# Kernel tuning notes

Measured on AMD Instinct MI355X. Metric: run time of the kernel, lower is better.

Reference implementation:

```python
import jax, jax.numpy as jnp
import numpy as np

V = 25000
E = 100000
NODE_IN = 74
EDGE_IN = 12
OUT = 64
EHID = 128
NUM_STEPS = 6


def setup_inputs() -> dict:
    key = jax.random.key(0)
    ks = jax.random.split(key, 12)
    s = 0.05
    node_feats = jax.random.normal(ks[0], (V, NODE_IN), dtype=jnp.float32)
    edge_feats = jax.random.normal(ks[1], (E, EDGE_IN), dtype=jnp.float32)
    src = jax.random.randint(ks[2], (E,), 0, V)
    dst = jax.random.randint(ks[3], (E,), 0, V)
    # project_node_feats: Linear(node_in, out)
    Wp = jax.random.normal(ks[4], (NODE_IN, OUT), dtype=jnp.float32) * s
    bp = jnp.zeros((OUT,), dtype=jnp.float32)
    # edge network: Linear(edge_in, ehid) -> ReLU -> Linear(ehid, out*out)
    We1 = jax.random.normal(ks[5], (EDGE_IN, EHID), dtype=jnp.float32) * s
    be1 = jnp.zeros((EHID,), dtype=jnp.float32)
    We2 = jax.random.normal(ks[6], (EHID, OUT * OUT), dtype=jnp.float32) * s
    be2 = jnp.zeros((OUT * OUT,), dtype=jnp.float32)
    # NNConv output bias
    bias = jnp.zeros((OUT,), dtype=jnp.float32)
    return {
        "node_feats": node_feats, "edge_feats": edge_feats,
        "src": src, "dst": dst,
        "Wp": Wp, "bp": bp,
        "We1": We1, "be1": be1, "We2": We2, "be2": be2,
        "bias": bias,
    }


def reference(node_feats, edge_feats, src, dst, Wp, bp, We1, be1, We2, be2, bias):
    # project node features
    h = jax.nn.relu(node_feats @ Wp + bp)  # [V, OUT]
    # per-edge weight matrices (same every step -> hoist out of loop)
    ew = jax.nn.relu(edge_feats @ We1 + be1) @ We2 + be2  # [E, OUT*OUT]
    ew = ew.reshape(E, OUT, OUT)
    for _ in range(NUM_STEPS):
        # gather src node feats, batched matvec, scatter-sum to dst
        msg = jnp.einsum('ei,eio->eo', h[src], ew)  # [E, OUT]
        agg = jax.ops.segment_sum(msg, dst, num_segments=V)  # [V, OUT]
        h = jax.nn.relu(agg + bias)
    return h
```

## Files before the change

### kernel.cpp

```cpp
#include <hip/hip_runtime.h>
#include <hip/hip_bf16.h>

#define Vn 25000
#define En 100000
#define NODE_IN 74
#define EDGE_IN 12
#define OUTD 64
#define EHID 128
#define NUM_STEPS 6

typedef __attribute__((ext_vector_type(8))) short short8;
typedef __attribute__((ext_vector_type(4))) float floatx4;

__device__ __forceinline__ short f2bfbits(float x) {
  union { float fv; unsigned u; } c; c.fv = x;
  unsigned r = (c.u + 0x7fffu + ((c.u >> 16) & 1u)) >> 16;
  return (short)r;
}

__global__ void proj_kernel(const float* __restrict__ node,
                            const float* __restrict__ Wp,
                            const float* __restrict__ bp,
                            float* __restrict__ h) {
  __shared__ float nf[NODE_IN];
  int v = blockIdx.x;
  int o = threadIdx.x;
  for (int i = o; i < NODE_IN; i += 64) nf[i] = node[(size_t)v * NODE_IN + i];
  __syncthreads();
  float acc = bp[o];
  for (int i = 0; i < NODE_IN; ++i) acc = fmaf(nf[i], Wp[i * OUTD + o], acc);
  h[(size_t)v * OUTD + o] = fmaxf(acc, 0.0f);
}

__global__ void edge_kernel(const float* __restrict__ ef,
                            const float* __restrict__ We1,
                            const float* __restrict__ be1,
                            __hip_bfloat16* __restrict__ f) {
  __shared__ float es[EDGE_IN];
  int e = blockIdx.x;
  int k = threadIdx.x;
  if (k < EDGE_IN) es[k] = ef[(size_t)e * EDGE_IN + k];
  __syncthreads();
  float acc = be1[k];
  for (int j = 0; j < EDGE_IN; ++j) acc = fmaf(es[j], We1[j * EHID + k], acc);
  f[(size_t)e * EHID + k] = __float2bfloat16(fmaxf(acc, 0.0f));
}

__global__ void w2r_kernel(const float* __restrict__ We2,
                           __hip_bfloat16* __restrict__ w2s) {
  int g = blockIdx.x * 256 + threadIdx.x;
  int j = g & 7;
  int quad = (g >> 3) & 3;
  int l15 = (g >> 5) & 15;
  int s = (g >> 9) & 3;
  int wv = (g >> 11) & 3;
  int i = g >> 13;
  int k = s * 32 + quad * 8 + j;
  int col = i * 64 + wv * 16 + l15;
  w2s[g] = __float2bfloat16(We2[(size_t)k * (OUTD * OUTD) + col]);
}

__global__ __launch_bounds__(256) void msg_kernel(
    const float* __restrict__ h,
    const __hip_bfloat16* __restrict__ f,
    const __hip_bfloat16* __restrict__ w2s,
    const int* __restrict__ src,
    const int* __restrict__ dst,
    const float* __restrict__ be2,
    float* __restrict__ agg) {
  __shared__ float h_t[64 * 68];
  __shared__ int s_dst[64];

  const int tid = threadIdx.x;
  const int wv = tid >> 6;
  const int lane = tid & 63;
  const int quad = lane >> 4;
  const int l15 = lane & 15;
  const int e0 = blockIdx.x * 64;

  if (tid < 64) {
    int e = e0 + tid;
    s_dst[tid] = (e < En) ? dst[e] : -1;
  }
  {
    int e = tid & 63;
    int ib = tid >> 6;
    int eg = e0 + e;
    int sv = (eg < En) ? src[eg] : 0;
    const float4* hp = reinterpret_cast<const float4*>(h + (size_t)sv * OUTD + ib * 16);
    for (int c = 0; c < 4; ++c) {
      float4 val = hp[c];
      int ib4 = ib * 16 + c * 4;
      h_t[(ib4 + 0) * 68 + e] = val.x;
      h_t[(ib4 + 1) * 68 + e] = val.y;
      h_t[(ib4 + 2) * 68 + e] = val.z;
      h_t[(ib4 + 3) * 68 + e] = val.w;
    }
  }
  __syncthreads();

  short8 afr[4][4];
  for (int t = 0; t < 4; ++t) {
    int e = e0 + t * 16 + l15;
    if (e >= En) e = En - 1;
    const short* fr = reinterpret_cast<const short*>(f) + (size_t)e * EHID + quad * 8;
    for (int s = 0; s < 4; ++s)
      afr[t][s] = *reinterpret_cast<const short8*>(fr + s * 32);
  }

  const short* w2b = reinterpret_cast<const short*>(w2s) +
                     wv * 2048 + l15 * 32 + quad * 8;

#define LOADB(dstv, ii)                                                     \
  {                                                                         \
    const short* p_ = w2b + (size_t)(ii) * 8192;                            \
    dstv[0] = *reinterpret_cast<const short8*>(p_);                         \
    dstv[1] = *reinterpret_cast<const short8*>(p_ + 512);                   \
    dstv[2] = *reinterpret_cast<const short8*>(p_ + 1024);                  \
    dstv[3] = *reinterpret_cast<const short8*>(p_ + 1536);                  \
  }

  floatx4 msgacc[4];
  const floatx4 zero4 = (floatx4){0.f, 0.f, 0.f, 0.f};
  for (int t = 0; t < 4; ++t) msgacc[t] = zero4;

  short8 ba[4], bb[4];
  LOADB(ba, 0);
  LOADB(bb, 1);

#define BODY(iv, breg)                                                         \
  {                                                                            \
    floatx4 hv[4];                                                             \
    for (int t = 0; t < 4; ++t)                                                \
      hv[t] = *reinterpret_cast<const floatx4*>(&h_t[(iv) * 68 + t * 16 + quad * 4]); \
    for (int t = 0; t < 4; ++t) {                                              \
      floatx4 c = __builtin_amdgcn_mfma_f32_16x16x32_bf16(afr[t][0], breg[0], zero4, 0, 0, 0); \
      c = __builtin_amdgcn_mfma_f32_16x16x32_bf16(afr[t][1], breg[1], c, 0, 0, 0); \
      c = __builtin_amdgcn_mfma_f32_16x16x32_bf16(afr[t][2], breg[2], c, 0, 0, 0); \
      c = __builtin_amdgcn_mfma_f32_16x16x32_bf16(afr[t][3], breg[3], c, 0, 0, 0); \
      msgacc[t] += c * hv[t];                                                  \
    }                                                                          \
  }

  for (int ii = 0; ii < 32; ++ii) {
    int i0 = 2 * ii;
    BODY(i0, ba);
    {
      int inx = (i0 + 2 < 64) ? i0 + 2 : 63;
      LOADB(ba, inx);
    }
    BODY(i0 + 1, bb);
    {
      int inx = (i0 + 3 < 64) ? i0 + 3 : 63;
      LOADB(bb, inx);
    }
  }

  {
    short8 b2f8[2];
    for (int s = 0; s < 2; ++s) {
      short8 v;
      for (int j = 0; j < 8; ++j)
        v[j] = f2bfbits(be2[(s * 32 + quad * 8 + j) * 64 + wv * 16 + l15]);
      b2f8[s] = v;
    }
    for (int t = 0; t < 4; ++t) {
      short8 ha[2];
      for (int s = 0; s < 2; ++s)
        for (int j = 0; j < 8; ++j)
          ha[s][j] = f2bfbits(h_t[(s * 32 + quad * 8 + j) * 68 + t * 16 + l15]);
      msgacc[t] = __builtin_amdgcn_mfma_f32_16x16x32_bf16(ha[0], b2f8[0], msgacc[t], 0, 0, 0);
      msgacc[t] = __builtin_amdgcn_mfma_f32_16x16x32_bf16(ha[1], b2f8[1], msgacc[t], 0, 0, 0);
    }
  }

  int col = wv * 16 + l15;
  for (int t = 0; t < 4; ++t) {
    int rb = t * 16 + quad * 4;
    for (int r = 0; r < 4; ++r) {
      int d = s_dst[rb + r];
      if (d >= 0) atomicAdd(&agg[(size_t)d * OUTD + col], msgacc[t][r]);
    }
  }
}

__global__ void update_kernel(float* __restrict__ agg,
                              const float* __restrict__ bias,
                              float* __restrict__ hout,
                              float* __restrict__ dout, int last) {
  int g = blockIdx.x * 256 + threadIdx.x;
  if (g >= Vn * OUTD) return;
  float v = agg[g];
  agg[g] = 0.0f;
  float r = fmaxf(v + bias[g & 63], 0.0f);
  hout[g] = r;
  if (last) dout[g] = r;
}

extern "C" void kernel_launch(void* const* d_in, const int* in_sizes, int n_in,
                              void* d_out, int out_size, void* d_ws, size_t ws_size,
                              hipStream_t stream) {
  const float* node = (const float*)d_in[0];
  const float* edge = (const float*)d_in[1];
  const int* src = (const int*)d_in[2];
  const int* dst = (const int*)d_in[3];
  const float* Wp   = (const float*)d_in[4];
  const float* bp   = (const float*)d_in[5];
  const float* We1  = (const float*)d_in[6];
  const float* be1  = (const float*)d_in[7];
  const float* We2  = (const float*)d_in[8];
  const float* be2  = (const float*)d_in[9];
  const float* bias = (const float*)d_in[10];
  float* out = (float*)d_out;

  char* ws = (char*)d_ws;
  float* agg = (float*)(ws);
  float* h_a = (float*)(ws + 6400000);
  float* h_b = (float*)(ws + 12800000);
  __hip_bfloat16* f   = (__hip_bfloat16*)(ws + 19200000);
  __hip_bfloat16* w2s = (__hip_bfloat16*)(ws + 44800000);

  hipMemsetAsync(agg, 0, (size_t)Vn * OUTD * sizeof(float), stream);
  proj_kernel<<<Vn, 64, 0, stream>>>(node, Wp, bp, h_a);
  edge_kernel<<<En, 128, 0, stream>>>(edge, We1, be1, f);
  w2r_kernel<<<(OUTD * OUTD * EHID) / 256, 256, 0, stream>>>(We2, w2s);

  float* hin = h_a;
  float* hout = h_b;
  for (int s = 0; s < NUM_STEPS; ++s) {
    msg_kernel<<<(En + 63) / 64, 256, 0, stream>>>(hin, f, w2s, src, dst, be2, agg);
    update_kernel<<<(Vn * OUTD + 255) / 256, 256, 0, stream>>>(
        agg, bias, hout, out, s == NUM_STEPS - 1);
    float* t = hin; hin = hout; hout = t;
  }
}
```

Baseline: 960.9 us.

## Split message kernel over input-dim halves to double block count

Each 64-edge block is split into two blocks, each handling half of the input dimension (32 of 64 i values), with its own partial sums atomically added to agg. This doubles the grid, halves shared memory per block and shortens the serial loop, aiming for better occupancy and latency hiding. In exchange the f-fragment loads, src/dst loads and atomicAdds to agg are all doubled, raising atomic traffic.

```diff
diff --git a/kernel.cpp b/kernel.cpp
--- a/kernel.cpp
+++ b/kernel.cpp
@@ -8,6 +8,8 @@
 #define OUTD 64
 #define EHID 128
 #define NUM_STEPS 6
+
+#define HPAD 68
 
 typedef __attribute__((ext_vector_type(8))) short short8;
 typedef __attribute__((ext_vector_type(4))) float floatx4;
@@ -68,7 +70,7 @@
     const int* __restrict__ dst,
     const float* __restrict__ be2,
     float* __restrict__ agg) {
-  __shared__ float h_t[64 * 68];
+  __shared__ float h_t[32 * HPAD];
   __shared__ int s_dst[64];
 
   const int tid = threadIdx.x;
@@ -76,7 +78,9 @@
   const int lane = tid & 63;
   const int quad = lane >> 4;
   const int l15 = lane & 15;
-  const int e0 = blockIdx.x * 64;
+  const int eb = blockIdx.x >> 1;
+  const int ih = blockIdx.x & 1;
+  const int e0 = eb * 64;
 
   if (tid < 64) {
     int e = e0 + tid;
@@ -87,14 +91,15 @@
     int ib = tid >> 6;
     int eg = e0 + e;
     int sv = (eg < En) ? src[eg] : 0;
-    const float4* hp = reinterpret_cast<const float4*>(h + (size_t)sv * OUTD + ib * 16);
-    for (int c = 0; c < 4; ++c) {
+    const float4* hp = reinterpret_cast<const float4*>(
+        h + (size_t)sv * OUTD + ih * 32 + ib * 8);
+    for (int c = 0; c < 2; ++c) {
       float4 val = hp[c];
-      int ib4 = ib * 16 + c * 4;
-      h_t[(ib4 + 0) * 68 + e] = val.x;
-      h_t[(ib4 + 1) * 68 + e] = val.y;
-      h_t[(ib4 + 2) * 68 + e] = val.z;
-      h_t[(ib4 + 3) * 68 + e] = val.w;
+      int il = ib * 8 + c * 4;
+      h_t[(il + 0) * HPAD + e] = val.x;
+      h_t[(il + 1) * HPAD + e] = val.y;
+      h_t[(il + 2) * HPAD + e] = val.z;
+      h_t[(il + 3) * HPAD + e] = val.w;
     }
   }
   __syncthreads();
@@ -125,52 +130,45 @@
   for (int t = 0; t < 4; ++t) msgacc[t] = zero4;
 
   short8 ba[4], bb[4];
-  LOADB(ba, 0);
-  LOADB(bb, 1);
-
-#define BODY(iv, breg)                                                         \
+  LOADB(ba, ih * 32 + 0);
+  LOADB(bb, ih * 32 + 1);
+
+#define BODY(il, breg)                                                         \
   {                                                                            \
-    floatx4 hv[4];                                                             \
-    for (int t = 0; t < 4; ++t)                                                \
-      hv[t] = *reinterpret_cast<const floatx4*>(&h_t[(iv) * 68 + t * 16 + quad * 4]); \
     for (int t = 0; t < 4; ++t) {                                              \
+      floatx4 hv = *reinterpret_cast<const floatx4*>(                          \
+          &h_t[(il) * HPAD + t * 16 + quad * 4]);                              \
       floatx4 c = __builtin_amdgcn_mfma_f32_16x16x32_bf16(afr[t][0], breg[0], zero4, 0, 0, 0); \
       c = __builtin_amdgcn_mfma_f32_16x16x32_bf16(afr[t][1], breg[1], c, 0, 0, 0); \
       c = __builtin_amdgcn_mfma_f32_16x16x32_bf16(afr[t][2], breg[2], c, 0, 0, 0); \
       c = __builtin_amdgcn_mfma_f32_16x16x32_bf16(afr[t][3], breg[3], c, 0, 0, 0); \
-      msgacc[t] += c * hv[t];                                                  \
+      msgacc[t] += c * hv;                                                     \
     }                                                                          \
   }
 
-  for (int ii = 0; ii < 32; ++ii) {
-    int i0 = 2 * ii;
-    BODY(i0, ba);
+  for (int ii = 0; ii < 16; ++ii) {
+    int il0 = 2 * ii;
+    BODY(il0, ba);
     {
-      int inx = (i0 + 2 < 64) ? i0 + 2 : 63;
-      LOADB(ba, inx);
-    }
-    BODY(i0 + 1, bb);
+      int inx = (il0 + 2 < 32) ? il0 + 2 : 31;
+      LOADB(ba, ih * 32 + inx);
+    }
+    BODY(il0 + 1, bb);
     {
-      int inx = (i0 + 3 < 64) ? i0 + 3 : 63;
-      LOADB(bb, inx);
+      int inx = (il0 + 3 < 32) ? il0 + 3 : 31;
+      LOADB(bb, ih * 32 + inx);
     }
   }
 
   {
-    short8 b2f8[2];
-    for (int s = 0; s < 2; ++s) {
-      short8 v;
+    short8 b2f8;
+    for (int j = 0; j < 8; ++j)
+      b2f8[j] = f2bfbits(be2[(ih * 32 + quad * 8 + j) * 64 + wv * 16 + l15]);
+    for (int t = 0; t < 4; ++t) {
+      short8 ha;
       for (int j = 0; j < 8; ++j)
-        v[j] = f2bfbits(be2[(s * 32 + quad * 8 + j) * 64 + wv * 16 + l15]);
-      b2f8[s] = v;
-    }
-    for (int t = 0; t < 4; ++t) {
-      short8 ha[2];
-      for (int s = 0; s < 2; ++s)
-        for (int j = 0; j < 8; ++j)
-          ha[s][j] = f2bfbits(h_t[(s * 32 + quad * 8 + j) * 68 + t * 16 + l15]);
-      msgacc[t] = __builtin_amdgcn_mfma_f32_16x16x32_bf16(ha[0], b2f8[0], msgacc[t], 0, 0, 0);
-      msgacc[t] = __builtin_amdgcn_mfma_f32_16x16x32_bf16(ha[1], b2f8[1], msgacc[t], 0, 0, 0);
+        ha[j] = f2bfbits(h_t[(quad * 8 + j) * HPAD + t * 16 + l15]);
+      msgacc[t] = __builtin_amdgcn_mfma_f32_16x16x32_bf16(ha, b2f8, msgacc[t], 0, 0, 0);
     }
   }
 
@@ -225,10 +223,11 @@
   edge_kernel<<<En, 128, 0, stream>>>(edge, We1, be1, f);
   w2r_kernel<<<(OUTD * OUTD * EHID) / 256, 256, 0, stream>>>(We2, w2s);
 
+  int nblk = ((En + 63) / 64) * 2;
   float* hin = h_a;
   float* hout = h_b;
   for (int s = 0; s < NUM_STEPS; ++s) {
-    msg_kernel<<<(En + 63) / 64, 256, 0, stream>>>(hin, f, w2s, src, dst, be2, agg);
+    msg_kernel<<<nblk, 256, 0, stream>>>(hin, f, w2s, src, dst, be2, agg);
     update_kernel<<<(Vn * OUTD + 255) / 256, 256, 0, stream>>>(
         agg, bias, hout, out, s == NUM_STEPS - 1);
     float* t = hin; hin = hout; hout = t;
```

After: 946.4 us. Within noise of the previous version (-1.5%).

## Fold h scaling into fp16 A operand and chain MFMA accumulation directly

Applied to the files above, without the earlier changes.

Switches the bf16 datapath to fp16 and changes how the per-edge h value is applied. Before, it was a per-output-row scale of each 16x16x32 MFMA result followed by a vector multiply-add. Now h is multiplied into the A fragment with packed fp16 ops, so all MFMAs accumulate straight into msgacc. This removes the zero-init partial chains and the float4 FMA per step, and lets MFMAs chain without dependent VALU. The cost is 4 packed half multiplies per MFMA and fp16 rounding of h and of f*h, which risks precision or overflow.

```diff
diff --git a/kernel.cpp b/kernel.cpp
--- a/kernel.cpp
+++ b/kernel.cpp
@@ -9,14 +9,10 @@
 #define EHID 128
 #define NUM_STEPS 6
 
-typedef __attribute__((ext_vector_type(8))) short short8;
+#define HPAD 68
+
+typedef __attribute__((ext_vector_type(8))) _Float16 half8;
 typedef __attribute__((ext_vector_type(4))) float floatx4;
-
-__device__ __forceinline__ short f2bfbits(float x) {
-  union { float fv; unsigned u; } c; c.fv = x;
-  unsigned r = (c.u + 0x7fffu + ((c.u >> 16) & 1u)) >> 16;
-  return (short)r;
-}
 
 __global__ void proj_kernel(const float* __restrict__ node,
                             const float* __restrict__ Wp,
@@ -35,7 +31,7 @@
 __global__ void edge_kernel(const float* __restrict__ ef,
                             const float* __restrict__ We1,
                             const float* __restrict__ be1,
-                            __hip_bfloat16* __restrict__ f) {
+                            _Float16* __restrict__ f) {
   __shared__ float es[EDGE_IN];
   int e = blockIdx.x;
   int k = threadIdx.x;
@@ -43,11 +39,11 @@
   __syncthreads();
   float acc = be1[k];
   for (int j = 0; j < EDGE_IN; ++j) acc = fmaf(es[j], We1[j * EHID + k], acc);
-  f[(size_t)e * EHID + k] = __float2bfloat16(fmaxf(acc, 0.0f));
+  f[(size_t)e * EHID + k] = (_Float16)fmaxf(acc, 0.0f);
 }
 
 __global__ void w2r_kernel(const float* __restrict__ We2,
-                           __hip_bfloat16* __restrict__ w2s) {
+                           _Float16* __restrict__ w2s) {
   int g = blockIdx.x * 256 + threadIdx.x;
   int j = g & 7;
   int quad = (g >> 3) & 3;
@@ -57,18 +53,18 @@
   int i = g >> 13;
   int k = s * 32 + quad * 8 + j;
   int col = i * 64 + wv * 16 + l15;
-  w2s[g] = __float2bfloat16(We2[(size_t)k * (OUTD * OUTD) + col]);
+  w2s[g] = (_Float16)We2[(size_t)k * (OUTD * OUTD) + col];
 }
 
 __global__ __launch_bounds__(256) void msg_kernel(
     const float* __restrict__ h,
-    const __hip_bfloat16* __restrict__ f,
-    const __hip_bfloat16* __restrict__ w2s,
+    const _Float16* __restrict__ f,
+    const _Float16* __restrict__ w2s,
     const int* __restrict__ src,
     const int* __restrict__ dst,
     const float* __restrict__ be2,
     float* __restrict__ agg) {
-  __shared__ float h_t[64 * 68];
+  __shared__ float h_t[64 * HPAD];
   __shared__ int s_dst[64];
 
   const int tid = threadIdx.x;
@@ -90,56 +86,57 @@
     const float4* hp = reinterpret_cast<const float4*>(h + (size_t)sv * OUTD + ib * 16);
     for (int c = 0; c < 4; ++c) {
       float4 val = hp[c];
-      int ib4 = ib * 16 + c * 4;
-      h_t[(ib4 + 0) * 68 + e] = val.x;
-      h_t[(ib4 + 1) * 68 + e] = val.y;
-      h_t[(ib4 + 2) * 68 + e] = val.z;
-      h_t[(ib4 + 3) * 68 + e] = val.w;
+      int i4 = ib * 16 + c * 4;
+      h_t[(i4 + 0) * HPAD + e] = val.x;
+      h_t[(i4 + 1) * HPAD + e] = val.y;
+      h_t[(i4 + 2) * HPAD + e] = val.z;
+      h_t[(i4 + 3) * HPAD + e] = val.w;
     }
   }
   __syncthreads();
 
-  short8 afr[4][4];
+  half8 afr[4][4];
   for (int t = 0; t < 4; ++t) {
     int e = e0 + t * 16 + l15;
     if (e >= En) e = En - 1;
-    const short* fr = reinterpret_cast<const short*>(f) + (size_t)e * EHID + quad * 8;
+    const _Float16* fr = f + (size_t)e * EHID + quad * 8;
     for (int s = 0; s < 4; ++s)
-      afr[t][s] = *reinterpret_cast<const short8*>(fr + s * 32);
-  }
-
-  const short* w2b = reinterpret_cast<const short*>(w2s) +
-                     wv * 2048 + l15 * 32 + quad * 8;
+      afr[t][s] = *reinterpret_cast<const half8*>(fr + s * 32);
+  }
+
+  const _Float16* w2b = w2s + wv * 2048 + l15 * 32 + quad * 8;
 
 #define LOADB(dstv, ii)                                                     \
   {                                                                         \
-    const short* p_ = w2b + (size_t)(ii) * 8192;                            \
-    dstv[0] = *reinterpret_cast<const short8*>(p_);                         \
-    dstv[1] = *reinterpret_cast<const short8*>(p_ + 512);                   \
-    dstv[2] = *reinterpret_cast<const short8*>(p_ + 1024);                  \
-    dstv[3] = *reinterpret_cast<const short8*>(p_ + 1536);                  \
+    const _Float16* p_ = w2b + (size_t)(ii) * 8192;                         \
+    dstv[0] = *reinterpret_cast<const half8*>(p_);                          \
+    dstv[1] = *reinterpret_cast<const half8*>(p_ + 512);                    \
+    dstv[2] = *reinterpret_cast<const half8*>(p_ + 1024);                   \
+    dstv[3] = *reinterpret_cast<const half8*>(p_ + 1536);                   \
   }
 
   floatx4 msgacc[4];
   const floatx4 zero4 = (floatx4){0.f, 0.f, 0.f, 0.f};
   for (int t = 0; t < 4; ++t) msgacc[t] = zero4;
 
-  short8 ba[4], bb[4];
+  half8 ba[4], bb[4];
   LOADB(ba, 0);
   LOADB(bb, 1);
 
 #define BODY(iv, breg)                                                         \
   {                                                                            \
-    floatx4 hv[4];                                                             \
+    _Float16 hf[4];                                                            \
     for (int t = 0; t < 4; ++t)                                                \
-      hv[t] = *reinterpret_cast<const floatx4*>(&h_t[(iv) * 68 + t * 16 + quad * 4]); \
-    for (int t = 0; t < 4; ++t) {                                              \
-      floatx4 c = __builtin_amdgcn_mfma_f32_16x16x32_bf16(afr[t][0], breg[0], zero4, 0, 0, 0); \
-      c = __builtin_amdgcn_mfma_f32_16x16x32_bf16(afr[t][1], breg[1], c, 0, 0, 0); \
-      c = __builtin_amdgcn_mfma_f32_16x16x32_bf16(afr[t][2], breg[2], c, 0, 0, 0); \
-      c = __builtin_amdgcn_mfma_f32_16x16x32_bf16(afr[t][3], breg[3], c, 0, 0, 0); \
-      msgacc[t] += c * hv[t];                                                  \
-    }                                                                          \
+      hf[t] = (_Float16)h_t[(iv) * HPAD + t * 16 + l15];                       \
+    half8 hb[4];                                                               \
+    for (int t = 0; t < 4; ++t)                                                \
+      hb[t] = (half8){hf[t], hf[t], hf[t], hf[t], hf[t], hf[t], hf[t], hf[t]}; \
+    for (int s = 0; s < 4; ++s)                                                \
+      for (int t = 0; t < 4; ++t) {                                            \
+        half8 as = afr[t][s] * hb[t];                                          \
+        msgacc[t] = __builtin_amdgcn_mfma_f32_16x16x32_f16(as, breg[s],        \
+                                                           msgacc[t], 0, 0, 0); \
+      }                                                                        \
   }
 
   for (int ii = 0; ii < 32; ++ii) {
@@ -157,20 +154,20 @@
   }
 
   {
-    short8 b2f8[2];
+    half8 b2f8[2];
     for (int s = 0; s < 2; ++s) {
-      short8 v;
+      half8 v;
       for (int j = 0; j < 8; ++j)
-        v[j] = f2bfbits(be2[(s * 32 + quad * 8 + j) * 64 + wv * 16 + l15]);
+        v[j] = (_Float16)be2[(s * 32 + quad * 8 + j) * 64 + wv * 16 + l15];
       b2f8[s] = v;
     }
     for (int t = 0; t < 4; ++t) {
-      short8 ha[2];
+      half8 ha[2];
       for (int s = 0; s < 2; ++s)
         for (int j = 0; j < 8; ++j)
-          ha[s][j] = f2bfbits(h_t[(s * 32 + quad * 8 + j) * 68 + t * 16 + l15]);
-      msgacc[t] = __builtin_amdgcn_mfma_f32_16x16x32_bf16(ha[0], b2f8[0], msgacc[t], 0, 0, 0);
-      msgacc[t] = __builtin_amdgcn_mfma_f32_16x16x32_bf16(ha[1], b2f8[1], msgacc[t], 0, 0, 0);
+          ha[s][j] = (_Float16)h_t[(s * 32 + quad * 8 + j) * HPAD + t * 16 + l15];
+      msgacc[t] = __builtin_amdgcn_mfma_f32_16x16x32_f16(ha[0], b2f8[0], msgacc[t], 0, 0, 0);
+      msgacc[t] = __builtin_amdgcn_mfma_f32_16x16x32_f16(ha[1], b2f8[1], msgacc[t], 0, 0, 0);
     }
   }
 
@@ -217,8 +214,8 @@
   float* agg = (float*)(ws);
   float* h_a = (float*)(ws + 6400000);
   float* h_b = (float*)(ws + 12800000);
-  __hip_bfloat16* f   = (__hip_bfloat16*)(ws + 19200000);
-  __hip_bfloat16* w2s = (__hip_bfloat16*)(ws + 44800000);
+  _Float16* f   = (_Float16*)(ws + 19200000);
+  _Float16* w2s = (_Float16*)(ws + 44800000);
 
   hipMemsetAsync(agg, 0, (size_t)Vn * OUTD * sizeof(float), stream);
   proj_kernel<<<Vn, 64, 0, stream>>>(node, Wp, bp, h_a);
```

New measurement: 925.4 us. 3.7% less time.
